# Kernel optimization log

Measured on AMD Instinct MI355X. Metric: run time of the kernel, lower is better.

## Reference

```python
import jax, jax.numpy as jnp
import numpy as np

HEADS = 4
DIM_HEAD = 32
SCALE = 10.0
EPS = 1e-12

def l2norm_axis1(t):
    # Faithful to source: default axis=1 -> normalize over the SEQUENCE axis of [B,N,h,d]
    denom = jnp.clip(jnp.linalg.norm(t, ord=2, axis=1, keepdims=True), EPS)
    return t / denom

def setup_inputs() -> dict:
    key = jax.random.key(0)
    k1, k2, k3 = jax.random.split(key, 3)
    B, N, C = 4, 4096, 128
    dim = HEADS * DIM_HEAD  # 128
    x = jax.random.normal(k1, (B, N, C), dtype=jnp.float32)
    W_qkv = jax.random.normal(k2, (C, 3 * dim), dtype=jnp.float32) * (1.0 / np.sqrt(C))
    W_out = jax.random.normal(k3, (dim, C), dtype=jnp.float32) * (1.0 / np.sqrt(dim))
    b_out = jnp.zeros((C,), dtype=jnp.float32)
    return {"x": x, "W_qkv": W_qkv, "W_out": W_out, "b_out": b_out}

def reference(x, W_qkv, W_out, b_out):
    B, N, C = x.shape
    # 1x1 conv == per-token linear
    qkv = jnp.einsum('bnc,ce->bne', x, W_qkv)  # [B,N,3*dim]
    q, k, v = jnp.split(qkv, 3, axis=-1)
    # [B,N,h,d]
    q = q.reshape(B, N, HEADS, DIM_HEAD)
    k = k.reshape(B, N, HEADS, DIM_HEAD)
    v = v.reshape(B, N, HEADS, DIM_HEAD)
    q = l2norm_axis1(q)
    k = l2norm_axis1(k)
    sim = jnp.einsum('bihd,bjhd->bhij', q, k) * SCALE  # [B,h,N,N]
    attn = jax.nn.softmax(sim, axis=-1)
    out = jnp.einsum('bhij,bjhd->bhid', attn, v)  # [B,h,N,d]
    out = out.transpose(0, 2, 1, 3).reshape(B, N, HEADS * DIM_HEAD)  # [B,N,dim]
    return jnp.einsum('bne,ec->bnc', out, W_out) + b_out
```

## Files before the change

kernel.cpp:

```cpp
#include <hip/hip_runtime.h>

typedef short s16x8 __attribute__((ext_vector_type(8)));
typedef short s16x4 __attribute__((ext_vector_type(4)));
typedef float f32x4 __attribute__((ext_vector_type(4)));
typedef float f4 __attribute__((ext_vector_type(4)));
typedef unsigned short u16x4 __attribute__((ext_vector_type(4)));

#define CEXP 14.426950408889634074f

__device__ __forceinline__ unsigned short f2bf(float f) {
    union { float f; unsigned int i; } v; v.f = f;
    unsigned int x = v.i;
    return (unsigned short)((x + 0x7fffu + ((x >> 16) & 1u)) >> 16);
}
__device__ __forceinline__ float bf2f(unsigned short u) {
    union { unsigned int i; float f; } v; v.i = ((unsigned int)u) << 16; return v.f;
}

__device__ __forceinline__ s16x4 pk_bf16x4(float p0, float p1, float p2, float p3) {
#if __has_builtin(__builtin_amdgcn_cvt_pk_bf16_f32)
    typedef __bf16 bf16x2 __attribute__((ext_vector_type(2)));
    union { struct { bf16x2 a, b; } h; s16x4 s; } r;
    r.h.a = __builtin_amdgcn_cvt_pk_bf16_f32(p0, p1);
    r.h.b = __builtin_amdgcn_cvt_pk_bf16_f32(p2, p3);
    return r.s;
#else
    unsigned u0 = __float_as_uint(p0) + 0x8000u;
    unsigned u1 = __float_as_uint(p1) + 0x8000u;
    unsigned u2 = __float_as_uint(p2) + 0x8000u;
    unsigned u3 = __float_as_uint(p3) + 0x8000u;
    union { uint2 u; s16x4 s; } pb;
    pb.u.x = __builtin_amdgcn_perm(u1, u0, 0x07060302u);
    pb.u.y = __builtin_amdgcn_perm(u3, u2, 0x07060302u);
    return pb.s;
#endif
}

__device__ __forceinline__ u16x4 pk4(f4 v) {
    u16x4 r = { f2bf(v[0]), f2bf(v[1]), f2bf(v[2]), f2bf(v[3]) };
    return r;
}

__device__ __forceinline__ void gl_lds16(const void* g, void* l) {
    __builtin_amdgcn_global_load_lds(
        (const __attribute__((address_space(1))) void*)g,
        (__attribute__((address_space(3))) void*)l,
        16, 0, 0);
}

__global__ __launch_bounds__(256) void k_prep(
    const float* __restrict__ Wqkv, const float* __restrict__ Wout,
    unsigned short* __restrict__ Wt, unsigned short* __restrict__ WoT,
    float* __restrict__ sumsqp)
{
    __shared__ float tile[64][65];
    const int blk = blockIdx.x, tid = threadIdx.x;
    if (blk >= 16) {
        sumsqp[(blk - 16) * 256 + tid] = 0.f;
        return;
    }
    const float* src;
    unsigned short* dst;
    int lds_src, k0, n0;
    if (blk < 12) {
        src = Wqkv; dst = Wt; lds_src = 384;
        k0 = (blk & 1) * 64; n0 = (blk >> 1) * 64;
    } else {
        int b = blk - 12;
        src = Wout; dst = WoT; lds_src = 128;
        k0 = (b & 1) * 64; n0 = (b >> 1) * 64;
    }
    const int c = tid & 63, r0 = tid >> 6;
#pragma unroll
    for (int i = 0; i < 16; ++i) {
        int row = i * 4 + r0;
        tile[row][c] = src[(size_t)(k0 + row) * lds_src + n0 + c];
    }
    __syncthreads();
#pragma unroll
    for (int i = 0; i < 16; ++i) {
        int n = i * 4 + r0;
        dst[(size_t)(n0 + n) * 128 + k0 + c] = f2bf(tile[c][n]);
    }
}

__global__ __launch_bounds__(256, 2) void k_qkv(
    const float* __restrict__ x, const unsigned short* __restrict__ Wt,
    unsigned short* __restrict__ Qb, unsigned short* __restrict__ Kb,
    unsigned short* __restrict__ Vt, float* __restrict__ sumsqp)
{
    __shared__ float red[4][64];
    const int tid = threadIdx.x;
    const int wl = tid >> 6, lane = tid & 63;
    const int qd = lane >> 4, nn = lane & 15;
    const int yb = blockIdx.y;
    const int tw0 = blockIdx.x * 64 + wl * 16;

    const float* apf = x + (size_t)(tw0 + nn) * 128 + qd * 8;
    s16x8 af[4];
#pragma unroll
    for (int ks = 0; ks < 4; ++ks) {
        f4 a0 = *(const f4*)(apf + ks * 32);
        f4 a1 = *(const f4*)(apf + ks * 32 + 4);
        union { struct { s16x4 lo, hi; } h; s16x8 v; } u;
        u.h.lo = pk_bf16x4(a0[0], a0[1], a0[2], a0[3]);
        u.h.hi = pk_bf16x4(a1[0], a1[1], a1[2], a1[3]);
        af[ks] = u.v;
    }

    const int b = tw0 >> 12;
    const int tl0 = tw0 & 4095;
    const int tok = tl0 + nn;

#pragma unroll
    for (int c = 0; c < 2; ++c) {
        const int n0 = c * 128 + yb * 64;
        const unsigned short* bp = Wt + (size_t)(n0 + nn) * 128 + qd * 8;
        s16x8 bfr[16];
#pragma unroll
        for (int nb = 0; nb < 4; ++nb)
#pragma unroll
            for (int ks = 0; ks < 4; ++ks)
                bfr[nb * 4 + ks] = *(const s16x8*)(bp + (size_t)nb * 2048 + ks * 32);

        f32x4 acc[4];
#pragma unroll
        for (int nb = 0; nb < 4; ++nb) acc[nb] = (f32x4){0.f, 0.f, 0.f, 0.f};
#pragma unroll
        for (int ks = 0; ks < 4; ++ks)
#pragma unroll
            for (int nb = 0; nb < 4; ++nb)
                acc[nb] = __builtin_amdgcn_mfma_f32_16x16x32_bf16(bfr[nb * 4 + ks], af[ks], acc[nb], 0, 0, 0);

        unsigned short* dst = (c == 0) ? Qb : Kb;
#pragma unroll
        for (int nb = 0; nb < 4; ++nb) {
            const int dim = yb * 64 + nb * 16 + qd * 4;
            const int h = dim >> 5, d0 = dim & 31;
            *(u16x4*)&dst[(size_t)((b * 4 + h) * 4096 + tok) * 32 + d0] = pk4(acc[nb]);
            f32x4 ss;
#pragma unroll
            for (int r = 0; r < 4; ++r) ss[r] = acc[nb][r] * acc[nb][r];
#pragma unroll
            for (int m = 1; m < 16; m <<= 1) {
#pragma unroll
                for (int r = 0; r < 4; ++r) ss[r] += __shfl_xor(ss[r], m);
            }
            if (nn == 0)
                *(f4*)&red[wl][nb * 16 + qd * 4] = ss;
        }
        __syncthreads();
        if (tid < 64) {
            float s = red[0][tid] + red[1][tid] + red[2][tid] + red[3][tid];
            const int g = (c << 9) + (b << 7) + yb * 64 + tid;
            atomicAdd(&sumsqp[((blockIdx.x & 7) << 10) + g], s);
        }
        __syncthreads();
    }

    {
        const int n0 = 256 + yb * 64;
        const unsigned short* bp = Wt + (size_t)(n0 + nn) * 128 + qd * 8;
        s16x8 bfr[16];
#pragma unroll
        for (int nb = 0; nb < 4; ++nb)
#pragma unroll
            for (int ks = 0; ks < 4; ++ks)
                bfr[nb * 4 + ks] = *(const s16x8*)(bp + (size_t)nb * 2048 + ks * 32);

        f32x4 acc[4];
#pragma unroll
        for (int nb = 0; nb < 4; ++nb) acc[nb] = (f32x4){0.f, 0.f, 0.f, 0.f};
#pragma unroll
        for (int ks = 0; ks < 4; ++ks)
#pragma unroll
            for (int nb = 0; nb < 4; ++nb)
                acc[nb] = __builtin_amdgcn_mfma_f32_16x16x32_bf16(af[ks], bfr[nb * 4 + ks], acc[nb], 0, 0, 0);
#pragma unroll
        for (int nb = 0; nb < 4; ++nb) {
            const int dim = yb * 64 + nb * 16 + nn;
            const int h = dim >> 5, d = dim & 31;
            *(u16x4*)&Vt[(size_t)((b * 4 + h) * 32 + d) * 4096 + tl0 + qd * 4] = pk4(acc[nb]);
        }
    }
}

__global__ __launch_bounds__(512, 4) void k_attn(
    const unsigned short* __restrict__ Qb, const unsigned short* __restrict__ Kb,
    const unsigned short* __restrict__ Vt, const float* __restrict__ sumsqp,
    unsigned short* __restrict__ Ogb)
{
    __shared__ char smem[65536];
    const int tid  = threadIdx.x;
    const int wv   = tid >> 6, lane = tid & 63;
    const int wl   = wv & 3, half = wv >> 2;
    const int qd   = lane >> 4, nn = lane & 15;
    const int bh   = blockIdx.x;
    const int ib   = blockIdx.y * 128 + wl * 32;
    const unsigned short* Qbh = Qb + (size_t)bh * 4096 * 32;
    const unsigned short* Kbh = Kb + (size_t)bh * 4096 * 32;
    const unsigned short* Vbh = Vt + (size_t)bh * 32 * 4096;

    float rj[8];
    {
        const int gq = bh * 32 + qd * 8;
#pragma unroll
        for (int j = 0; j < 8; ++j) {
            float sq = 0.f, sk = 0.f;
#pragma unroll
            for (int c = 0; c < 8; ++c) {
                sq += sumsqp[c * 1024 + gq + j];
                sk += sumsqp[c * 1024 + 512 + gq + j];
            }
            rj[j] = fminf(__builtin_amdgcn_rsqf(sq), 1e12f)
                  * fminf(__builtin_amdgcn_rsqf(sk), 1e12f) * CEXP;
        }
    }

    s16x8 q0r = *(const s16x8*)(Qbh + (ib + nn) * 32 + qd * 8);
    s16x8 q1r = *(const s16x8*)(Qbh + (ib + 16 + nn) * 32 + qd * 8);
    s16x8 qf0, qf1;
#pragma unroll
    for (int j = 0; j < 8; ++j) {
        qf0[j] = (short)f2bf(bf2f((unsigned short)q0r[j]) * rj[j]);
        qf1[j] = (short)f2bf(bf2f((unsigned short)q1r[j]) * rj[j]);
    }

    f32x4 o00 = {0.f,0.f,0.f,0.f}, o01 = {0.f,0.f,0.f,0.f};
    f32x4 o10 = {0.f,0.f,0.f,0.f}, o11 = {0.f,0.f,0.f,0.f};
    f32x4 la  = {0.f,0.f,0.f,0.f}, lb  = {0.f,0.f,0.f,0.f};
    const f32x4 zro = {0.f,0.f,0.f,0.f};
    const s16x8 ones8 = { (short)0x3F80, (short)0x3F80, (short)0x3F80, (short)0x3F80,
                          (short)0x3F80, (short)0x3F80, (short)0x3F80, (short)0x3F80 };

    const int KB0 = half * 16384;
    const int VB0 = 32768 + half * 16384;
    const int jb0 = half * 2048;

    const int jperm = ((wl >> 1) << 5) + ((nn >> 2) << 3) + ((wl & 1) << 2) + (nn & 3);
    const unsigned short* ksrc = Kbh + (size_t)(jb0 + jperm) * 32 + qd * 8;
    const unsigned short* vsrc = Vbh + (size_t)((wl >> 1) * 16 + nn) * 4096
                               + jb0 + (wl & 1) * 32 + qd * 8;
    char* kbase = smem + KB0 + wl * 1024;
    char* vbase = smem + VB0 + wl * 1024;

    {
        gl_lds16(ksrc,        kbase);
        gl_lds16(ksrc + 2048, kbase + 4096);
        gl_lds16(vsrc,        vbase);
        gl_lds16(vsrc + 64,   vbase + 4096);
        ksrc += 4096; vsrc += 128;
    }

    for (int ph = 0; ph < 16; ++ph) {
        __syncthreads();
        if (ph < 15) {
            const int nxt = ((ph + 1) & 1) * 8192;
            gl_lds16(ksrc,        kbase + nxt);
            gl_lds16(ksrc + 2048, kbase + nxt + 4096);
            gl_lds16(vsrc,        vbase + nxt);
            gl_lds16(vsrc + 64,   vbase + nxt + 4096);
            ksrc += 4096; vsrc += 128;
        }
        const char* kslot = smem + KB0 + (ph & 1) * 8192;
        const char* vslot = smem + VB0 + (ph & 1) * 8192;
#pragma unroll
        for (int t = 0; t < 2; ++t) {
            const char* kcur = kslot + t * 4096;
            const char* vcur = vslot + t * 4096;
#pragma unroll
            for (int js32 = 0; js32 < 2; ++js32) {
                s16x8 kf0 = *(const s16x8*)(kcur + (js32 * 2 + 0) * 1024 + lane * 16);
                s16x8 kf1 = *(const s16x8*)(kcur + (js32 * 2 + 1) * 1024 + lane * 16);
                f32x4 sa0 = __builtin_amdgcn_mfma_f32_16x16x32_bf16(kf0, qf0, zro, 0, 0, 0);
                f32x4 sb0 = __builtin_amdgcn_mfma_f32_16x16x32_bf16(kf0, qf1, zro, 0, 0, 0);
                f32x4 sa1 = __builtin_amdgcn_mfma_f32_16x16x32_bf16(kf1, qf0, zro, 0, 0, 0);
                f32x4 sb1 = __builtin_amdgcn_mfma_f32_16x16x32_bf16(kf1, qf1, zro, 0, 0, 0);
                float a0 = __builtin_amdgcn_exp2f(sa0[0]);
                float a1 = __builtin_amdgcn_exp2f(sa0[1]);
                float a2 = __builtin_amdgcn_exp2f(sa0[2]);
                float a3 = __builtin_amdgcn_exp2f(sa0[3]);
                float a4 = __builtin_amdgcn_exp2f(sa1[0]);
                float a5 = __builtin_amdgcn_exp2f(sa1[1]);
                float a6 = __builtin_amdgcn_exp2f(sa1[2]);
                float a7 = __builtin_amdgcn_exp2f(sa1[3]);
                float b0 = __builtin_amdgcn_exp2f(sb0[0]);
                float b1 = __builtin_amdgcn_exp2f(sb0[1]);
                float b2 = __builtin_amdgcn_exp2f(sb0[2]);
                float b3 = __builtin_amdgcn_exp2f(sb0[3]);
                float b4 = __builtin_amdgcn_exp2f(sb1[0]);
                float b5 = __builtin_amdgcn_exp2f(sb1[1]);
                float b6 = __builtin_amdgcn_exp2f(sb1[2]);
                float b7 = __builtin_amdgcn_exp2f(sb1[3]);
                union { struct { s16x4 lo, hi; } h; s16x8 v; } ua, ub;
                ua.h.lo = pk_bf16x4(a0, a1, a2, a3);
                ua.h.hi = pk_bf16x4(a4, a5, a6, a7);
                ub.h.lo = pk_bf16x4(b0, b1, b2, b3);
                ub.h.hi = pk_bf16x4(b4, b5, b6, b7);
                s16x8 pa32 = ua.v, pb32 = ub.v;
                la = __builtin_amdgcn_mfma_f32_16x16x32_bf16(ones8, pa32, la, 0, 0, 0);
                lb = __builtin_amdgcn_mfma_f32_16x16x32_bf16(ones8, pb32, lb, 0, 0, 0);
                s16x8 va = *(const s16x8*)(vcur + js32 * 1024 + lane * 16);
                s16x8 vb = *(const s16x8*)(vcur + 2048 + js32 * 1024 + lane * 16);
                o00 = __builtin_amdgcn_mfma_f32_16x16x32_bf16(va, pa32, o00, 0, 0, 0);
                o01 = __builtin_amdgcn_mfma_f32_16x16x32_bf16(vb, pa32, o01, 0, 0, 0);
                o10 = __builtin_amdgcn_mfma_f32_16x16x32_bf16(va, pb32, o10, 0, 0, 0);
                o11 = __builtin_amdgcn_mfma_f32_16x16x32_bf16(vb, pb32, o11, 0, 0, 0);
            }
        }
    }

    const float lpa = la[0];
    const float lpb = lb[0];
    __syncthreads();
    float* Ob = (float*)smem;
    float* Lb = (float*)(smem + 16384);
    if (half) {
        float* d0 = Ob + ((wl * 2 + 0) * 64 + lane) * 8;
        *(f4*)d0 = o00; *(f4*)(d0 + 4) = o01;
        float* d1 = Ob + ((wl * 2 + 1) * 64 + lane) * 8;
        *(f4*)d1 = o10; *(f4*)(d1 + 4) = o11;
        Lb[(wl * 2 + 0) * 64 + lane] = lpa;
        Lb[(wl * 2 + 1) * 64 + lane] = lpb;
    }
    __syncthreads();
    if (!half) {
        const int bb = bh >> 2, hh = bh & 3;
        float* s0 = Ob + ((wl * 2 + 0) * 64 + lane) * 8;
        float rla = 1.f / (lpa + Lb[(wl * 2 + 0) * 64 + lane]);
        f4 m00 = (o00 + *(const f4*)s0) * rla;
        f4 m01 = (o01 + *(const f4*)(s0 + 4)) * rla;
        float* s1 = Ob + ((wl * 2 + 1) * 64 + lane) * 8;
        float rlb = 1.f / (lpb + Lb[(wl * 2 + 1) * 64 + lane]);
        f4 m10 = (o10 + *(const f4*)s1) * rlb;
        f4 m11 = (o11 + *(const f4*)(s1 + 4)) * rlb;
        unsigned short* dst0 = Ogb + (size_t)(bb * 4096 + blockIdx.y * 128 + wl * 32 + nn) * 128
                             + hh * 32 + qd * 4;
        *(u16x4*)dst0 = pk4(m00);
        *(u16x4*)(dst0 + 16) = pk4(m01);
        unsigned short* dst1 = dst0 + (size_t)16 * 128;
        *(u16x4*)dst1 = pk4(m10);
        *(u16x4*)(dst1 + 16) = pk4(m11);
    }
}

__global__ __launch_bounds__(256, 2) void k_out(
    const unsigned short* __restrict__ Ogb, const unsigned short* __restrict__ WoT,
    const float* __restrict__ bout, float* __restrict__ out)
{
    const int tid = threadIdx.x;
    const int wl = tid >> 6, lane = tid & 63;
    const int qd = lane >> 4, nn = lane & 15;
    const int n0 = blockIdx.y * 64;
    const int tw0 = blockIdx.x * 64 + wl * 16;

    const unsigned short* ap = WoT + (size_t)(n0 + nn) * 128 + qd * 8;
    const unsigned short* bp = Ogb + (size_t)(tw0 + nn) * 128 + qd * 8;
    s16x8 bfr[4], afr[16];
#pragma unroll
    for (int ks = 0; ks < 4; ++ks) bfr[ks] = *(const s16x8*)(bp + ks * 32);
#pragma unroll
    for (int nb = 0; nb < 4; ++nb)
#pragma unroll
        for (int ks = 0; ks < 4; ++ks)
            afr[nb * 4 + ks] = *(const s16x8*)(ap + (size_t)nb * 2048 + ks * 32);

    f32x4 acc[4];
#pragma unroll
    for (int nb = 0; nb < 4; ++nb) acc[nb] = (f32x4){0.f, 0.f, 0.f, 0.f};
#pragma unroll
    for (int ks = 0; ks < 4; ++ks)
#pragma unroll
        for (int nb = 0; nb < 4; ++nb)
            acc[nb] = __builtin_amdgcn_mfma_f32_16x16x32_bf16(afr[nb * 4 + ks], bfr[ks], acc[nb], 0, 0, 0);

#pragma unroll
    for (int nb = 0; nb < 4; ++nb) {
        const int c = n0 + nb * 16 + qd * 4;
        f4 bv = *(const f4*)&bout[c];
        f4 r;
#pragma unroll
        for (int j = 0; j < 4; ++j) r[j] = acc[nb][j] + bv[j];
        *(f4*)&out[(size_t)(tw0 + nn) * 128 + c] = r;
    }
}

extern "C" void kernel_launch(void* const* d_in, const int* in_sizes, int n_in,
                              void* d_out, int out_size, void* d_ws, size_t ws_size,
                              hipStream_t stream)
{
    const float* x    = (const float*)d_in[0];
    const float* Wqkv = (const float*)d_in[1];
    const float* Wout = (const float*)d_in[2];
    const float* bout = (const float*)d_in[3];
    float* out = (float*)d_out;
    char* ws = (char*)d_ws;
    const size_t MB = 1024 * 1024;
    unsigned short* Qb  = (unsigned short*)(ws);
    unsigned short* Kb  = (unsigned short*)(ws + 4 * MB);
    unsigned short* Vt  = (unsigned short*)(ws + 8 * MB);
    unsigned short* Ogb = (unsigned short*)(ws + 12 * MB);
    unsigned short* Wt  = (unsigned short*)(ws + 16 * MB);
    unsigned short* WoT = (unsigned short*)(ws + 16 * MB + 112 * 1024);
    float*       sumsqp = (float*)(ws + 16 * MB + 160 * 1024);

    hipLaunchKernelGGL(k_prep, dim3(48), dim3(256), 0, stream, Wqkv, Wout, Wt, WoT, sumsqp);
    hipLaunchKernelGGL(k_qkv, dim3(256, 2), dim3(256), 0, stream, x, Wt, Qb, Kb, Vt, sumsqp);
    hipLaunchKernelGGL(k_attn, dim3(16, 32), dim3(512), 0, stream, Qb, Kb, Vt, sumsqp, Ogb);
    hipLaunchKernelGGL(k_out, dim3(256, 2), dim3(256), 0, stream, Ogb, WoT, bout, out);
}
```

Baseline: 141.7 us.

## Software-pipeline QK MFMA with previous step's exp and PV accumulation

Restructures the attention inner loop so each step issues the QK^T MFMAs for the current key block while doing the exp2, bf16 packing and PV/row-sum MFMAs for the previous block. V fragments are loaded one step ahead and carried in registers, and a final drain step runs after the loop. The goal is to hide MFMA result latency behind transcendental and packing work. In exchange it holds more live registers, which could lower occupancy. It also spends one dummy step whose -1e30 scores make exp2 return zero, so that step adds nothing to the sums.

```diff
diff --git a/kernel.cpp b/kernel.cpp
--- a/kernel.cpp
+++ b/kernel.cpp
@@ -233,6 +233,57 @@
     const s16x8 ones8 = { (short)0x3F80, (short)0x3F80, (short)0x3F80, (short)0x3F80,
                           (short)0x3F80, (short)0x3F80, (short)0x3F80, (short)0x3F80 };
 
+    f32x4 sa0p = {-1e30f,-1e30f,-1e30f,-1e30f};
+    f32x4 sa1p = {-1e30f,-1e30f,-1e30f,-1e30f};
+    f32x4 sb0p = {-1e30f,-1e30f,-1e30f,-1e30f};
+    f32x4 sb1p = {-1e30f,-1e30f,-1e30f,-1e30f};
+    s16x8 vap = {0,0,0,0,0,0,0,0};
+    s16x8 vbp = {0,0,0,0,0,0,0,0};
+
+#define FINISH_PREV() do {                                                    \
+    float a0 = __builtin_amdgcn_exp2f(sa0p[0]);                               \
+    float a1 = __builtin_amdgcn_exp2f(sa0p[1]);                               \
+    float a2 = __builtin_amdgcn_exp2f(sa0p[2]);                               \
+    float a3 = __builtin_amdgcn_exp2f(sa0p[3]);                               \
+    float a4 = __builtin_amdgcn_exp2f(sa1p[0]);                               \
+    float a5 = __builtin_amdgcn_exp2f(sa1p[1]);                               \
+    float a6 = __builtin_amdgcn_exp2f(sa1p[2]);                               \
+    float a7 = __builtin_amdgcn_exp2f(sa1p[3]);                               \
+    float b0 = __builtin_amdgcn_exp2f(sb0p[0]);                               \
+    float b1 = __builtin_amdgcn_exp2f(sb0p[1]);                               \
+    float b2 = __builtin_amdgcn_exp2f(sb0p[2]);                               \
+    float b3 = __builtin_amdgcn_exp2f(sb0p[3]);                               \
+    float b4 = __builtin_amdgcn_exp2f(sb1p[0]);                               \
+    float b5 = __builtin_amdgcn_exp2f(sb1p[1]);                               \
+    float b6 = __builtin_amdgcn_exp2f(sb1p[2]);                               \
+    float b7 = __builtin_amdgcn_exp2f(sb1p[3]);                               \
+    union { struct { s16x4 lo, hi; } h; s16x8 v; } ua, ub;                    \
+    ua.h.lo = pk_bf16x4(a0, a1, a2, a3);                                      \
+    ua.h.hi = pk_bf16x4(a4, a5, a6, a7);                                      \
+    ub.h.lo = pk_bf16x4(b0, b1, b2, b3);                                      \
+    ub.h.hi = pk_bf16x4(b4, b5, b6, b7);                                      \
+    s16x8 pa32 = ua.v, pb32 = ub.v;                                           \
+    la  = __builtin_amdgcn_mfma_f32_16x16x32_bf16(ones8, pa32, la, 0, 0, 0);  \
+    lb  = __builtin_amdgcn_mfma_f32_16x16x32_bf16(ones8, pb32, lb, 0, 0, 0);  \
+    o00 = __builtin_amdgcn_mfma_f32_16x16x32_bf16(vap, pa32, o00, 0, 0, 0);   \
+    o01 = __builtin_amdgcn_mfma_f32_16x16x32_bf16(vbp, pa32, o01, 0, 0, 0);   \
+    o10 = __builtin_amdgcn_mfma_f32_16x16x32_bf16(vap, pb32, o10, 0, 0, 0);   \
+    o11 = __builtin_amdgcn_mfma_f32_16x16x32_bf16(vbp, pb32, o11, 0, 0, 0);   \
+} while (0)
+
+#define ATTN_STEP(kc, vc, js) do {                                            \
+    s16x8 kf0 = *(const s16x8*)((kc) + ((js) * 2 + 0) * 1024 + lane * 16);    \
+    s16x8 kf1 = *(const s16x8*)((kc) + ((js) * 2 + 1) * 1024 + lane * 16);    \
+    s16x8 van = *(const s16x8*)((vc) + (js) * 1024 + lane * 16);              \
+    s16x8 vbn = *(const s16x8*)((vc) + 2048 + (js) * 1024 + lane * 16);       \
+    FINISH_PREV();                                                            \
+    sa0p = __builtin_amdgcn_mfma_f32_16x16x32_bf16(kf0, qf0, zro, 0, 0, 0);   \
+    sb0p = __builtin_amdgcn_mfma_f32_16x16x32_bf16(kf0, qf1, zro, 0, 0, 0);   \
+    sa1p = __builtin_amdgcn_mfma_f32_16x16x32_bf16(kf1, qf0, zro, 0, 0, 0);   \
+    sb1p = __builtin_amdgcn_mfma_f32_16x16x32_bf16(kf1, qf1, zro, 0, 0, 0);   \
+    vap = van; vbp = vbn;                                                     \
+} while (0)
+
     const int KB0 = half * 16384;
     const int VB0 = 32768 + half * 16384;
     const int jb0 = half * 2048;
@@ -264,51 +315,15 @@
         }
         const char* kslot = smem + KB0 + (ph & 1) * 8192;
         const char* vslot = smem + VB0 + (ph & 1) * 8192;
-#pragma unroll
-        for (int t = 0; t < 2; ++t) {
-            const char* kcur = kslot + t * 4096;
-            const char* vcur = vslot + t * 4096;
-#pragma unroll
-            for (int js32 = 0; js32 < 2; ++js32) {
-                s16x8 kf0 = *(const s16x8*)(kcur + (js32 * 2 + 0) * 1024 + lane * 16);
-                s16x8 kf1 = *(const s16x8*)(kcur + (js32 * 2 + 1) * 1024 + lane * 16);
-                f32x4 sa0 = __builtin_amdgcn_mfma_f32_16x16x32_bf16(kf0, qf0, zro, 0, 0, 0);
-                f32x4 sb0 = __builtin_amdgcn_mfma_f32_16x16x32_bf16(kf0, qf1, zro, 0, 0, 0);
-                f32x4 sa1 = __builtin_amdgcn_mfma_f32_16x16x32_bf16(kf1, qf0, zro, 0, 0, 0);
-                f32x4 sb1 = __builtin_amdgcn_mfma_f32_16x16x32_bf16(kf1, qf1, zro, 0, 0, 0);
-                float a0 = __builtin_amdgcn_exp2f(sa0[0]);
-                float a1 = __builtin_amdgcn_exp2f(sa0[1]);
-                float a2 = __builtin_amdgcn_exp2f(sa0[2]);
-                float a3 = __builtin_amdgcn_exp2f(sa0[3]);
-                float a4 = __builtin_amdgcn_exp2f(sa1[0]);
-                float a5 = __builtin_amdgcn_exp2f(sa1[1]);
-                float a6 = __builtin_amdgcn_exp2f(sa1[2]);
-                float a7 = __builtin_amdgcn_exp2f(sa1[3]);
-                float b0 = __builtin_amdgcn_exp2f(sb0[0]);
-                float b1 = __builtin_amdgcn_exp2f(sb0[1]);
-                float b2 = __builtin_amdgcn_exp2f(sb0[2]);
-                float b3 = __builtin_amdgcn_exp2f(sb0[3]);
-                float b4 = __builtin_amdgcn_exp2f(sb1[0]);
-                float b5 = __builtin_amdgcn_exp2f(sb1[1]);
-                float b6 = __builtin_amdgcn_exp2f(sb1[2]);
-                float b7 = __builtin_amdgcn_exp2f(sb1[3]);
-                union { struct { s16x4 lo, hi; } h; s16x8 v; } ua, ub;
-                ua.h.lo = pk_bf16x4(a0, a1, a2, a3);
-                ua.h.hi = pk_bf16x4(a4, a5, a6, a7);
-                ub.h.lo = pk_bf16x4(b0, b1, b2, b3);
-                ub.h.hi = pk_bf16x4(b4, b5, b6, b7);
-                s16x8 pa32 = ua.v, pb32 = ub.v;
-                la = __builtin_amdgcn_mfma_f32_16x16x32_bf16(ones8, pa32, la, 0, 0, 0);
-                lb = __builtin_amdgcn_mfma_f32_16x16x32_bf16(ones8, pb32, lb, 0, 0, 0);
-                s16x8 va = *(const s16x8*)(vcur + js32 * 1024 + lane * 16);
-                s16x8 vb = *(const s16x8*)(vcur + 2048 + js32 * 1024 + lane * 16);
-                o00 = __builtin_amdgcn_mfma_f32_16x16x32_bf16(va, pa32, o00, 0, 0, 0);
-                o01 = __builtin_amdgcn_mfma_f32_16x16x32_bf16(vb, pa32, o01, 0, 0, 0);
-                o10 = __builtin_amdgcn_mfma_f32_16x16x32_bf16(va, pb32, o10, 0, 0, 0);
-                o11 = __builtin_amdgcn_mfma_f32_16x16x32_bf16(vb, pb32, o11, 0, 0, 0);
-            }
-        }
-    }
+        ATTN_STEP(kslot,        vslot,        0);
+        ATTN_STEP(kslot,        vslot,        1);
+        ATTN_STEP(kslot + 4096, vslot + 4096, 0);
+        ATTN_STEP(kslot + 4096, vslot + 4096, 1);
+    }
+    FINISH_PREV();
+
+#undef ATTN_STEP
+#undef FINISH_PREV
 
     const float lpa = la[0];
     const float lpb = lb[0];
```

Result: no change. 141.6 us (-0.1%).
